# Optimization experiments

Hardware: AMD Instinct MI355X
Metric: run time of the kernel (lower is better)

Reference implementation:

```python
import jax, jax.numpy as jnp
import numpy as np

N = 50000      # nodes
E = 800000     # edges (before self-loops)
IN = 256       # in_dim
HID = 64       # hidden_dim per head
HEADS = 4
OUT = 256      # out_dim
NEG_SLOPE = 0.2


def setup_inputs() -> dict:
    key = jax.random.key(0)
    ks = jax.random.split(key, 12)
    s = 0.1
    return {
        "x": jax.random.normal(ks[0], (N, IN), jnp.float32),
        "edge_index": jax.random.randint(ks[1], (2, E), 0, N, dtype=jnp.int32),
        # layer 1: GATConv(IN, HID, heads=HEADS, concat=True)
        "W1": jax.random.normal(ks[2], (IN, HEADS * HID), jnp.float32) * s,
        "att_src1": jax.random.normal(ks[3], (HEADS, HID), jnp.float32) * s,
        "att_dst1": jax.random.normal(ks[4], (HEADS, HID), jnp.float32) * s,
        "b1": jnp.zeros((HEADS * HID,), jnp.float32),
        # layer 2: GATConv(HEADS*HID, OUT, heads=1, concat=False)
        "W2": jax.random.normal(ks[5], (HEADS * HID, OUT), jnp.float32) * s,
        "att_src2": jax.random.normal(ks[6], (1, OUT), jnp.float32) * s,
        "att_dst2": jax.random.normal(ks[7], (1, OUT), jnp.float32) * s,
        "b2": jnp.zeros((OUT,), jnp.float32),
    }


def _gat_layer(x, src, dst, W, a_src, a_dst, b, heads, concat):
    n = x.shape[0]
    h = (x @ W).reshape(n, heads, -1)                     # [N,H,F]
    al_s = jnp.einsum('nhf,hf->nh', h, a_src)             # [N,H]
    al_d = jnp.einsum('nhf,hf->nh', h, a_dst)
    e = jax.nn.leaky_relu(al_s[src] + al_d[dst], NEG_SLOPE)  # [E,H]
    # segment softmax over incoming edges of each dst node
    m = jax.lax.stop_gradient(jax.ops.segment_max(e, dst, num_segments=n))
    ex = jnp.exp(e - m[dst])
    denom = jax.ops.segment_sum(ex, dst, num_segments=n)
    alpha = ex / (denom[dst] + 1e-16)                     # [E,H]
    out = jax.ops.segment_sum(h[src] * alpha[:, :, None], dst, num_segments=n)  # [N,H,F]
    out = out.reshape(n, -1) if concat else out.mean(axis=1)
    return out + b


def reference(x, edge_index, W1, att_src1, att_dst1, b1, W2, att_src2, att_dst2, b2):
    n = x.shape[0]
    loop = jnp.arange(n, dtype=edge_index.dtype)
    ei = jnp.concatenate([edge_index, jnp.stack([loop, loop])], axis=1)  # add self loops
    src, dst = ei[0], ei[1]
    h = _gat_layer(x, src, dst, W1, att_src1, att_dst1, b1, HEADS, True)
    h = jax.nn.elu(h)
    out = _gat_layer(h, src, dst, W2, att_src2, att_dst2, b2, 1, False)
    return out
```

## Files before the change

kernel.cpp:

```cpp
#include <hip/hip_runtime.h>
#include <math.h>

#define IN_DIM 256
#define FDIM 256
#define HEADS 4
#define NEG 0.2f
#define MAXD 96

typedef __attribute__((ext_vector_type(8))) short bf16x8;
typedef __attribute__((ext_vector_type(8))) unsigned short u16x8;
typedef __attribute__((ext_vector_type(4))) float f32x4;

__device__ __forceinline__ float leaky(float x){ return x > 0.f ? x : NEG * x; }

__device__ __forceinline__ unsigned short f2bf(float f){
  unsigned int u = __float_as_uint(f);
  unsigned int r = u + 0x7fffu + ((u >> 16) & 1u);
  return (unsigned short)(r >> 16);
}
__device__ __forceinline__ float bf2f(unsigned short s){
  return __uint_as_float(((unsigned int)s) << 16);
}

__device__ __forceinline__ float4 bcast4(float4 v){
  return make_float4(__shfl(v.x,0,64), __shfl(v.y,0,64), __shfl(v.z,0,64), __shfl(v.w,0,64));
}
__device__ __forceinline__ float comp4(float4 v, int h){
  return h==0 ? v.x : h==1 ? v.y : h==2 ? v.z : v.w;
}

__device__ __forceinline__ void gld_lds16(const void* g, void* l){
  __builtin_amdgcn_global_load_lds((const __attribute__((address_space(1))) unsigned int*)g,
                                   (__attribute__((address_space(3))) unsigned int*)l, 16, 0, 0);
}

__global__ void k_hist(const int* __restrict__ dst, int* deg, int E){
  int e = blockIdx.x * blockDim.x + threadIdx.x;
  if (e < E) atomicAdd(&deg[dst[e]], 1);
}

__global__ void k_scanA(const int* __restrict__ deg, int* tmp, int* partials, int n){
  __shared__ int sm[256];
  int i = blockIdx.x * 256 + threadIdx.x;
  int v = (i < n) ? deg[i] + 1 : 0;
  sm[threadIdx.x] = v; __syncthreads();
  for (int off = 1; off < 256; off <<= 1){
    int x = (threadIdx.x >= off) ? sm[threadIdx.x - off] : 0;
    __syncthreads();
    sm[threadIdx.x] += x;
    __syncthreads();
  }
  if (i < n) tmp[i] = sm[threadIdx.x];
  if (threadIdx.x == 255) partials[blockIdx.x] = sm[255];
}

__global__ void k_scanB(int* partials, int nb){
  __shared__ int sm[1024];
  int t = threadIdx.x;
  int v = (t < nb) ? partials[t] : 0;
  sm[t] = v; __syncthreads();
  for (int off = 1; off < 1024; off <<= 1){
    int x = (t >= off) ? sm[t - off] : 0;
    __syncthreads();
    sm[t] += x;
    __syncthreads();
  }
  if (t < nb) partials[t] = sm[t] - v;
}

__global__ void k_scanC(const int* __restrict__ tmp, const int* __restrict__ deg,
                        const int* __restrict__ partials, int* rowptr, int n){
  int i = blockIdx.x * blockDim.x + threadIdx.x;
  if (i < n){
    int incl = tmp[i] + partials[i >> 8];
    rowptr[i] = incl - (deg[i] + 1);
    if (i == n - 1) rowptr[n] = incl;
  }
}

__global__ void k_fill(const int* __restrict__ src, const int* __restrict__ dst,
                       const int* __restrict__ rowptr, int* fill, int* col, int E, int n){
  int e = blockIdx.x * blockDim.x + threadIdx.x;
  if (e < E + n){
    int s, d;
    if (e < E){ s = src[e]; d = dst[e]; } else { s = d = e - E; }
    int pos = atomicAdd(&fill[d], 1);
    col[rowptr[d] + pos] = s;
  }
}

__global__ void k_castwt(const float* __restrict__ x, unsigned short* __restrict__ xb, int M, int castBlocks,
                         const float* __restrict__ W1, unsigned short* __restrict__ W1t,
                         const float* __restrict__ W2, unsigned short* __restrict__ W2t){
  int b = blockIdx.x;
  if (b < castBlocks){
    int idx = b * 256 + threadIdx.x;
    int row = idx >> 6;
    float4 v = make_float4(0.f, 0.f, 0.f, 0.f);
    if (row < M) v = *(const float4*)(x + (size_t)idx * 4);
    ushort4 o;
    o.x = f2bf(v.x); o.y = f2bf(v.y); o.z = f2bf(v.z); o.w = f2bf(v.w);
    *(ushort4*)(xb + (size_t)idx * 4) = o;
  } else {
    int bb = b - castBlocks;
    const float* W = (bb < 256) ? W1 : W2;
    unsigned short* Wt = (bb < 256) ? W1t : W2t;
    int nn = bb & 255, k = threadIdx.x;
    Wt[nn * 256 + k] = f2bf(W[k * 256 + nn]);
  }
}

__global__ __launch_bounds__(256) void k_gemm(const unsigned short* __restrict__ A,
                                              const unsigned short* __restrict__ Bt,
                                              unsigned short* __restrict__ C){
  __shared__ __align__(16) unsigned short sh[8192];
  unsigned short* As = sh;
  unsigned short* Bs = sh + 4096;
  int tid = threadIdx.x;
  int lane = tid & 63, wave = tid >> 6;
  int rowBase = blockIdx.x * 128, colBase = blockIdx.y * 128;
  int wr = (wave & 1) * 64, wc = (wave >> 1) * 64;

  f32x4 acc[4][4] = {};
  int c0 = tid, c1 = tid + 256;
  int r0 = c0 >> 2, kc0 = (c0 & 3) * 8;
  int r1 = c1 >> 2, kc1 = (c1 & 3) * 8;
  int m0 = lane & 15, kq = (lane >> 4) * 8;

  for (int k0 = 0; k0 < 256; k0 += 32){
    gld_lds16(A  + (size_t)(rowBase + r0) * 256 + k0 + kc0, (char*)As + c0 * 16);
    gld_lds16(A  + (size_t)(rowBase + r1) * 256 + k0 + kc1, (char*)As + c1 * 16);
    gld_lds16(Bt + (size_t)(colBase + r0) * 256 + k0 + kc0, (char*)Bs + c0 * 16);
    gld_lds16(Bt + (size_t)(colBase + r1) * 256 + k0 + kc1, (char*)Bs + c1 * 16);
    __syncthreads();
    bf16x8 af[4], bfr[4];
    #pragma unroll
    for (int it = 0; it < 4; ++it)
      af[it] = *(const bf16x8*)(As + (wr + it * 16 + m0) * 32 + kq);
    #pragma unroll
    for (int jt = 0; jt < 4; ++jt)
      bfr[jt] = *(const bf16x8*)(Bs + (wc + jt * 16 + m0) * 32 + kq);
    #pragma unroll
    for (int it = 0; it < 4; ++it)
      #pragma unroll
      for (int jt = 0; jt < 4; ++jt)
        acc[it][jt] = __builtin_amdgcn_mfma_f32_16x16x32_bf16(af[it], bfr[jt], acc[it][jt], 0, 0, 0);
    __syncthreads();
  }
  int cq = lane >> 4, cm = lane & 15;
  #pragma unroll
  for (int p = 0; p < 2; ++p){
    if ((wave >> 1) == p){
      #pragma unroll
      for (int it = 0; it < 4; ++it)
        #pragma unroll
        for (int jt = 0; jt < 4; ++jt)
          #pragma unroll
          for (int r = 0; r < 4; ++r)
            sh[(wr + it * 16 + cq * 4 + r) * 64 + jt * 16 + cm] = f2bf(acc[it][jt][r]);
    }
    __syncthreads();
    #pragma unroll
    for (int q = 0; q < 4; ++q){
      int id = tid + q * 256;
      int r = id >> 3, sg = id & 7;
      u16x8 v = *(const u16x8*)(sh + r * 64 + sg * 8);
      *(u16x8*)(C + (size_t)(rowBase + r) * 256 + colBase + p * 64 + sg * 8) = v;
    }
    __syncthreads();
  }
}

__global__ __launch_bounds__(256) void k_al4(const unsigned short* __restrict__ Hb,
                      const float* __restrict__ as_, const float* __restrict__ ad_,
                      float* als, float* ald, int n){
  int wave = threadIdx.x >> 6, lane = threadIdx.x & 63;
  int i = blockIdx.x * 4 + wave; if (i >= n) i = n - 1;
  int f = lane * 4;
  ushort4 hv = *(const ushort4*)(Hb + (size_t)i * FDIM + f);
  float4 av = *(const float4*)(as_ + f);
  float4 dv = *(const float4*)(ad_ + f);
  float h0 = bf2f(hv.x), h1 = bf2f(hv.y), h2 = bf2f(hv.z), h3 = bf2f(hv.w);
  float ps = h0*av.x + h1*av.y + h2*av.z + h3*av.w;
  float pd = h0*dv.x + h1*dv.y + h2*dv.z + h3*dv.w;
  #pragma unroll
  for (int off = 8; off >= 1; off >>= 1){
    ps += __shfl_down(ps, off, 16);
    pd += __shfl_down(pd, off, 16);
  }
  if ((lane & 15) == 0){
    int h = lane >> 4;
    als[i * HEADS + h] = ps; ald[i * HEADS + h] = pd;
  }
}

__global__ __launch_bounds__(256) void k_al1(const unsigned short* __restrict__ Hb,
                      const float* __restrict__ as_, const float* __restrict__ ad_,
                      float* als, float* ald, int n){
  int wave = threadIdx.x >> 6, lane = threadIdx.x & 63;
  int i = blockIdx.x * 4 + wave; if (i >= n) i = n - 1;
  int f = lane * 4;
  ushort4 hv = *(const ushort4*)(Hb + (size_t)i * FDIM + f);
  float4 av = *(const float4*)(as_ + f);
  float4 dv = *(const float4*)(ad_ + f);
  float h0 = bf2f(hv.x), h1 = bf2f(hv.y), h2 = bf2f(hv.z), h3 = bf2f(hv.w);
  float ps = h0*av.x + h1*av.y + h2*av.z + h3*av.w;
  float pd = h0*dv.x + h1*dv.y + h2*dv.z + h3*dv.w;
  #pragma unroll
  for (int off = 32; off >= 1; off >>= 1){
    ps += __shfl_down(ps, off, 64);
    pd += __shfl_down(pd, off, 64);
  }
  if (lane == 0){ als[i] = ps; ald[i] = pd; }
}

__global__ __launch_bounds__(256) void k_agg1(const unsigned short* __restrict__ Hb,
    const float* __restrict__ als, const float* __restrict__ ald,
    const int* __restrict__ rowptr, const int* __restrict__ col,
    const float* __restrict__ b, unsigned short* __restrict__ outb, int n){
  __shared__ __align__(16) int   colS[4][MAXD];
  __shared__ __align__(16) float wS[4][MAXD][4];
  int wave = threadIdx.x >> 6, t = threadIdx.x & 63;
  int i = blockIdx.x * 4 + wave; if (i >= n) i = n - 1;
  int start = rowptr[i];
  int deg = rowptr[i + 1] - start;
  float4 adv = *(const float4*)(ald + (size_t)i * 4);
  bool staged = (deg <= MAXD);

  float4 ls = make_float4(0.f, 0.f, 0.f, 0.f);
  if (staged){
    for (int j = t; j < deg; j += 64){
      int s = col[start + j];
      colS[wave][j] = s;
      float4 a = *(const float4*)(als + (size_t)s * 4);
      float4 w = make_float4(__expf(leaky(a.x + adv.x)), __expf(leaky(a.y + adv.y)),
                             __expf(leaky(a.z + adv.z)), __expf(leaky(a.w + adv.w)));
      *(float4*)(&wS[wave][j][0]) = w;
      ls.x += w.x; ls.y += w.y; ls.z += w.z; ls.w += w.w;
    }
  } else {
    for (int j = t; j < deg; j += 64){
      int s = col[start + j];
      float4 a = *(const float4*)(als + (size_t)s * 4);
      ls.x += __expf(leaky(a.x + adv.x)); ls.y += __expf(leaky(a.y + adv.y));
      ls.z += __expf(leaky(a.z + adv.z)); ls.w += __expf(leaky(a.w + adv.w));
    }
  }
  #pragma unroll
  for (int off = 32; off >= 1; off >>= 1) ls = make_float4(
      ls.x + __shfl_down(ls.x, off, 64), ls.y + __shfl_down(ls.y, off, 64),
      ls.z + __shfl_down(ls.z, off, 64), ls.w + __shfl_down(ls.w, off, 64));
  float4 d4 = bcast4(ls);
  __syncthreads();

  int e2 = t >> 5, l32 = t & 31;
  int h = l32 >> 3, f = l32 * 8;
  float inv = 1.f / (comp4(d4, h) + 1e-16f);
  const unsigned short* Hrow = Hb + f;
  float a0[8] = {0,0,0,0,0,0,0,0}, a1[8] = {0,0,0,0,0,0,0,0};
  if (staged){
    int j = 0;
    for (; j + 3 < deg; j += 4){
      int j0 = j + e2, j1 = j + 2 + e2;
      int s0 = colS[wave][j0], s1 = colS[wave][j1];
      float w0 = wS[wave][j0][h], w1 = wS[wave][j1][h];
      u16x8 h0 = *(const u16x8*)(Hrow + (size_t)s0 * FDIM);
      u16x8 h1 = *(const u16x8*)(Hrow + (size_t)s1 * FDIM);
      #pragma unroll
      for (int k = 0; k < 8; ++k){ a0[k] += bf2f(h0[k]) * w0; a1[k] += bf2f(h1[k]) * w1; }
    }
    for (; j < deg; j += 2){
      int jj = j + e2;
      if (jj < deg){
        int s = colS[wave][jj]; float w = wS[wave][jj][h];
        u16x8 hh = *(const u16x8*)(Hrow + (size_t)s * FDIM);
        #pragma unroll
        for (int k = 0; k < 8; ++k) a0[k] += bf2f(hh[k]) * w;
      }
    }
  } else {
    float adh = comp4(adv, h);
    for (int j = e2; j < deg; j += 2){
      int s = col[start + j];
      float w = __expf(leaky(als[(size_t)s * 4 + h] + adh));
      u16x8 hh = *(const u16x8*)(Hrow + (size_t)s * FDIM);
      #pragma unroll
      for (int k = 0; k < 8; ++k) a0[k] += bf2f(hh[k]) * w;
    }
  }
  float r[8];
  #pragma unroll
  for (int k = 0; k < 8; ++k){
    r[k] = a0[k] + a1[k];
    r[k] += __shfl_down(r[k], 32, 64);
  }
  if (t < 32){
    float4 bA = *(const float4*)(b + f);
    float4 bB = *(const float4*)(b + f + 4);
    float bb[8] = {bA.x, bA.y, bA.z, bA.w, bB.x, bB.y, bB.z, bB.w};
    u16x8 o;
    #pragma unroll
    for (int k = 0; k < 8; ++k){
      float v = r[k] * inv + bb[k];
      v = (v > 0.f) ? v : (__expf(v) - 1.f);
      o[k] = f2bf(v);
    }
    *(u16x8*)(outb + (size_t)i * FDIM + f) = o;
  }
}

__global__ __launch_bounds__(256) void k_agg2(const unsigned short* __restrict__ Hb,
    const float* __restrict__ als, const float* __restrict__ ald,
    const int* __restrict__ rowptr, const int* __restrict__ col,
    const float* __restrict__ b, float* __restrict__ out, int n){
  __shared__ __align__(16) int   colS[4][MAXD];
  __shared__ __align__(16) float wS[4][MAXD];
  int wave = threadIdx.x >> 6, t = threadIdx.x & 63;
  int i = blockIdx.x * 4 + wave; if (i >= n) i = n - 1;
  int start = rowptr[i];
  int deg = rowptr[i + 1] - start;
  float adv = ald[i];
  bool staged = (deg <= MAXD);

  float ls = 0.f;
  if (staged){
    for (int j = t; j < deg; j += 64){
      int s = col[start + j];
      colS[wave][j] = s;
      float w = __expf(leaky(als[s] + adv));
      wS[wave][j] = w;
      ls += w;
    }
  } else {
    for (int j = t; j < deg; j += 64) ls += __expf(leaky(als[col[start + j]] + adv));
  }
  #pragma unroll
  for (int off = 32; off >= 1; off >>= 1) ls += __shfl_down(ls, off, 64);
  float inv = 1.f / (__shfl(ls, 0, 64) + 1e-16f);
  __syncthreads();

  int e2 = t >> 5, l32 = t & 31;
  int f = l32 * 8;
  const unsigned short* Hrow = Hb + f;
  float a0[8] = {0,0,0,0,0,0,0,0}, a1[8] = {0,0,0,0,0,0,0,0};
  if (staged){
    int j = 0;
    for (; j + 3 < deg; j += 4){
      int j0 = j + e2, j1 = j + 2 + e2;
      int s0 = colS[wave][j0], s1 = colS[wave][j1];
      float w0 = wS[wave][j0], w1 = wS[wave][j1];
      u16x8 h0 = *(const u16x8*)(Hrow + (size_t)s0 * FDIM);
      u16x8 h1 = *(const u16x8*)(Hrow + (size_t)s1 * FDIM);
      #pragma unroll
      for (int k = 0; k < 8; ++k){ a0[k] += bf2f(h0[k]) * w0; a1[k] += bf2f(h1[k]) * w1; }
    }
    for (; j < deg; j += 2){
      int jj = j + e2;
      if (jj < deg){
        int s = colS[wave][jj]; float w = wS[wave][jj];
        u16x8 hh = *(const u16x8*)(Hrow + (size_t)s * FDIM);
        #pragma unroll
        for (int k = 0; k < 8; ++k) a0[k] += bf2f(hh[k]) * w;
      }
    }
  } else {
    for (int j = e2; j < deg; j += 2){
      int s = col[start + j];
      float w = __expf(leaky(als[s] + adv));
      u16x8 hh = *(const u16x8*)(Hrow + (size_t)s * FDIM);
      #pragma unroll
      for (int k = 0; k < 8; ++k) a0[k] += bf2f(hh[k]) * w;
    }
  }
  float r[8];
  #pragma unroll
  for (int k = 0; k < 8; ++k){
    r[k] = a0[k] + a1[k];
    r[k] += __shfl_down(r[k], 32, 64);
  }
  if (t < 32){
    float4 bA = *(const float4*)(b + f);
    float4 bB = *(const float4*)(b + f + 4);
    float4 oA = make_float4(r[0]*inv + bA.x, r[1]*inv + bA.y, r[2]*inv + bA.z, r[3]*inv + bA.w);
    float4 oB = make_float4(r[4]*inv + bB.x, r[5]*inv + bB.y, r[6]*inv + bB.z, r[7]*inv + bB.w);
    *(float4*)(out + (size_t)i * FDIM + f) = oA;
    *(float4*)(out + (size_t)i * FDIM + f + 4) = oB;
  }
}

extern "C" void kernel_launch(void* const* d_in, const int* in_sizes, int n_in,
                              void* d_out, int out_size, void* d_ws, size_t ws_size,
                              hipStream_t stream){
  const float* x   = (const float*)d_in[0];
  const int*   ei  = (const int*)d_in[1];
  const float* W1  = (const float*)d_in[2];
  const float* as1 = (const float*)d_in[3];
  const float* ad1 = (const float*)d_in[4];
  const float* b1  = (const float*)d_in[5];
  const float* W2  = (const float*)d_in[6];
  const float* as2 = (const float*)d_in[7];
  const float* ad2 = (const float*)d_in[8];
  const float* b2  = (const float*)d_in[9];
  float* out = (float*)d_out;

  int n = in_sizes[0] / IN_DIM;
  int E = in_sizes[1] / 2;
  int Mpad = (n + 127) & ~127;
  const int* srcIdx = ei;
  const int* dstIdx = ei + E;

  char* ws = (char*)d_ws;
  size_t off = 0;
  auto alloc = [&](size_t bytes) -> void* {
    void* p = ws + off; off += (bytes + 255) & ~(size_t)255; return p;
  };
  unsigned short* bufA = (unsigned short*)alloc((size_t)Mpad * FDIM * 2);
  unsigned short* bufB = (unsigned short*)alloc((size_t)Mpad * FDIM * 2);
  unsigned short* W1t  = (unsigned short*)alloc(256 * 256 * 2);
  unsigned short* W2t  = (unsigned short*)alloc(256 * 256 * 2);
  int*   tmp      = (int*)alloc((size_t)n * 4);
  int*   deg      = (int*)alloc((size_t)n * 4);
  int*   fill     = (int*)alloc((size_t)n * 4);
  int*   rowptr   = (int*)alloc((size_t)(n + 1) * 4);
  int*   partials = (int*)alloc(1024 * 4);
  int*   col      = (int*)alloc((size_t)(E + n) * 4);
  float* als1     = (float*)alloc((size_t)n * HEADS * 4);
  float* ald1     = (float*)alloc((size_t)n * HEADS * 4);
  float* als2     = (float*)alloc((size_t)n * 4);
  float* ald2     = (float*)alloc((size_t)n * 4);
  (void)ws_size;

  int nb = (n + 255) / 256;
  hipMemsetAsync(deg, 0, (size_t)n * 4, stream);
  hipMemsetAsync(fill, 0, (size_t)n * 4, stream);
  k_hist<<<(E + 255) / 256, 256, 0, stream>>>(dstIdx, deg, E);
  k_scanA<<<nb, 256, 0, stream>>>(deg, tmp, partials, n);
  k_scanB<<<1, 1024, 0, stream>>>(partials, nb);
  k_scanC<<<nb, 256, 0, stream>>>(tmp, deg, partials, rowptr, n);
  k_fill<<<(E + n + 255) / 256, 256, 0, stream>>>(srcIdx, dstIdx, rowptr, fill, col, E, n);

  int castBlocks = (Mpad * (FDIM / 4) + 255) / 256;
  k_castwt<<<castBlocks + 512, 256, 0, stream>>>(x, bufA, n, castBlocks, W1, W1t, W2, W2t);

  dim3 gg(Mpad / 128, FDIM / 128);
  int ga = (n + 3) / 4;
  k_gemm<<<gg, 256, 0, stream>>>(bufA, W1t, bufB);
  k_al4<<<ga, 256, 0, stream>>>(bufB, as1, ad1, als1, ald1, n);
  k_agg1<<<ga, 256, 0, stream>>>(bufB, als1, ald1, rowptr, col, b1, bufA, n);
  k_gemm<<<gg, 256, 0, stream>>>(bufA, W2t, bufB);
  k_al1<<<ga, 256, 0, stream>>>(bufB, as2, ad2, als2, ald2, n);
  k_agg2<<<ga, 256, 0, stream>>>(bufB, als2, ald2, rowptr, col, b2, out, n);
}
```

Measured before the change: 393.1 us.

## Fuse CSR build into cooperative kernel, fold attention logits into GEMM, unroll aggregation

```diff
diff --git a/kernel.cpp b/kernel.cpp
--- a/kernel.cpp
+++ b/kernel.cpp
@@ -1,5 +1,8 @@
 #include <hip/hip_runtime.h>
+#include <hip/hip_cooperative_groups.h>
 #include <math.h>
+
+namespace cg = cooperative_groups;
 
 #define IN_DIM 256
 #define FDIM 256
@@ -34,54 +37,82 @@
                                    (__attribute__((address_space(3))) unsigned int*)l, 16, 0, 0);
 }
 
-__global__ void k_hist(const int* __restrict__ dst, int* deg, int E){
-  int e = blockIdx.x * blockDim.x + threadIdx.x;
-  if (e < E) atomicAdd(&deg[dst[e]], 1);
-}
-
-__global__ void k_scanA(const int* __restrict__ deg, int* tmp, int* partials, int n){
+__global__ void k_coop(const float* __restrict__ x, unsigned short* __restrict__ xb,
+                       int castUnits, int M,
+                       const float* __restrict__ W1, unsigned short* __restrict__ W1t,
+                       const float* __restrict__ W2, unsigned short* __restrict__ W2t,
+                       const int* __restrict__ src, const int* __restrict__ dst, int E, int n,
+                       int* deg, int* fill, int* tmp, int* partials, int* rowptr, int* col,
+                       float* als2, float* ald2){
+  cg::grid_group grid = cg::this_grid();
   __shared__ int sm[256];
-  int i = blockIdx.x * 256 + threadIdx.x;
-  int v = (i < n) ? deg[i] + 1 : 0;
-  sm[threadIdx.x] = v; __syncthreads();
-  for (int off = 1; off < 256; off <<= 1){
-    int x = (threadIdx.x >= off) ? sm[threadIdx.x - off] : 0;
-    __syncthreads();
-    sm[threadIdx.x] += x;
-    __syncthreads();
-  }
-  if (i < n) tmp[i] = sm[threadIdx.x];
-  if (threadIdx.x == 255) partials[blockIdx.x] = sm[255];
-}
-
-__global__ void k_scanB(int* partials, int nb){
-  __shared__ int sm[1024];
   int t = threadIdx.x;
-  int v = (t < nb) ? partials[t] : 0;
-  sm[t] = v; __syncthreads();
-  for (int off = 1; off < 1024; off <<= 1){
-    int x = (t >= off) ? sm[t - off] : 0;
-    __syncthreads();
-    sm[t] += x;
-    __syncthreads();
-  }
-  if (t < nb) partials[t] = sm[t] - v;
-}
-
-__global__ void k_scanC(const int* __restrict__ tmp, const int* __restrict__ deg,
-                        const int* __restrict__ partials, int* rowptr, int n){
-  int i = blockIdx.x * blockDim.x + threadIdx.x;
-  if (i < n){
+  int gt = blockIdx.x * 256 + t;
+  const int GSZ = 256 * 256;
+  int nb = (n + 255) >> 8;
+
+  for (int i = gt; i < n; i += GSZ){ deg[i] = 0; fill[i] = 0; als2[i] = 0.f; ald2[i] = 0.f; }
+  for (int u = gt; u < castUnits; u += GSZ){
+    int row = u >> 6;
+    float4 v = make_float4(0.f, 0.f, 0.f, 0.f);
+    if (row < M) v = *(const float4*)(x + (size_t)u * 4);
+    ushort4 o;
+    o.x = f2bf(v.x); o.y = f2bf(v.y); o.z = f2bf(v.z); o.w = f2bf(v.w);
+    *(ushort4*)(xb + (size_t)u * 4) = o;
+  }
+  for (int u = gt; u < 2 * 65536; u += GSZ){
+    const float* W = (u < 65536) ? W1 : W2;
+    unsigned short* Wt = (u < 65536) ? W1t : W2t;
+    int e = u & 65535;
+    int k = e >> 8, nn = e & 255;
+    Wt[nn * 256 + k] = f2bf(W[k * 256 + nn]);
+  }
+  __threadfence();
+  grid.sync();
+
+  for (int e = gt; e < E; e += GSZ) atomicAdd(&deg[dst[e]], 1);
+  __threadfence();
+  grid.sync();
+
+  if (blockIdx.x < nb){
+    int i = blockIdx.x * 256 + t;
+    int v = (i < n) ? deg[i] + 1 : 0;
+    sm[t] = v; __syncthreads();
+    for (int off = 1; off < 256; off <<= 1){
+      int xv = (t >= off) ? sm[t - off] : 0;
+      __syncthreads();
+      sm[t] += xv;
+      __syncthreads();
+    }
+    if (i < n) tmp[i] = sm[t];
+    if (t == 255) partials[blockIdx.x] = sm[255];
+  }
+  __threadfence();
+  grid.sync();
+
+  if (blockIdx.x == 0){
+    int v = (t < nb) ? partials[t] : 0;
+    sm[t] = v; __syncthreads();
+    for (int off = 1; off < 256; off <<= 1){
+      int xv = (t >= off) ? sm[t - off] : 0;
+      __syncthreads();
+      sm[t] += xv;
+      __syncthreads();
+    }
+    if (t < nb) partials[t] = sm[t] - v;
+  }
+  __threadfence();
+  grid.sync();
+
+  for (int i = gt; i < n; i += GSZ){
     int incl = tmp[i] + partials[i >> 8];
     rowptr[i] = incl - (deg[i] + 1);
     if (i == n - 1) rowptr[n] = incl;
   }
-}
-
-__global__ void k_fill(const int* __restrict__ src, const int* __restrict__ dst,
-                       const int* __restrict__ rowptr, int* fill, int* col, int E, int n){
-  int e = blockIdx.x * blockDim.x + threadIdx.x;
-  if (e < E + n){
+  __threadfence();
+  grid.sync();
+
+  for (int e = gt; e < E + n; e += GSZ){
     int s, d;
     if (e < E){ s = src[e]; d = dst[e]; } else { s = d = e - E; }
     int pos = atomicAdd(&fill[d], 1);
@@ -89,30 +120,12 @@
   }
 }
 
-__global__ void k_castwt(const float* __restrict__ x, unsigned short* __restrict__ xb, int M, int castBlocks,
-                         const float* __restrict__ W1, unsigned short* __restrict__ W1t,
-                         const float* __restrict__ W2, unsigned short* __restrict__ W2t){
-  int b = blockIdx.x;
-  if (b < castBlocks){
-    int idx = b * 256 + threadIdx.x;
-    int row = idx >> 6;
-    float4 v = make_float4(0.f, 0.f, 0.f, 0.f);
-    if (row < M) v = *(const float4*)(x + (size_t)idx * 4);
-    ushort4 o;
-    o.x = f2bf(v.x); o.y = f2bf(v.y); o.z = f2bf(v.z); o.w = f2bf(v.w);
-    *(ushort4*)(xb + (size_t)idx * 4) = o;
-  } else {
-    int bb = b - castBlocks;
-    const float* W = (bb < 256) ? W1 : W2;
-    unsigned short* Wt = (bb < 256) ? W1t : W2t;
-    int nn = bb & 255, k = threadIdx.x;
-    Wt[nn * 256 + k] = f2bf(W[k * 256 + nn]);
-  }
-}
-
+template<int L>
 __global__ __launch_bounds__(256) void k_gemm(const unsigned short* __restrict__ A,
                                               const unsigned short* __restrict__ Bt,
-                                              unsigned short* __restrict__ C){
+                                              unsigned short* __restrict__ C,
+                                              const float* __restrict__ avS, const float* __restrict__ avD,
+                                              float* __restrict__ als, float* __restrict__ ald, int nvalid){
   __shared__ __align__(16) unsigned short sh[8192];
   unsigned short* As = sh;
   unsigned short* Bs = sh + 4096;
@@ -160,6 +173,34 @@
             sh[(wr + it * 16 + cq * 4 + r) * 64 + jt * 16 + cm] = f2bf(acc[it][jt][r]);
     }
     __syncthreads();
+    {
+      int r = tid >> 1, half = tid & 1;
+      int rg = rowBase + r;
+      const float* aS;
+      const float* aD;
+      if (L == 1){ aS = avS + (blockIdx.y * 2 + p) * 64; aD = avD + (blockIdx.y * 2 + p) * 64; }
+      else       { aS = avS + colBase + p * 64;          aD = avD + colBase + p * 64; }
+      float ps = 0.f, pd = 0.f;
+      #pragma unroll
+      for (int k4 = 0; k4 < 8; ++k4){
+        ushort4 hv = *(const ushort4*)(sh + r * 64 + half * 32 + k4 * 4);
+        float4 a4 = *(const float4*)(aS + half * 32 + k4 * 4);
+        float4 d4 = *(const float4*)(aD + half * 32 + k4 * 4);
+        ps += bf2f(hv.x)*a4.x + bf2f(hv.y)*a4.y + bf2f(hv.z)*a4.z + bf2f(hv.w)*a4.w;
+        pd += bf2f(hv.x)*d4.x + bf2f(hv.y)*d4.y + bf2f(hv.z)*d4.z + bf2f(hv.w)*d4.w;
+      }
+      ps += __shfl_xor(ps, 1, 64);
+      pd += __shfl_xor(pd, 1, 64);
+      if (half == 0 && rg < nvalid){
+        if (L == 1){
+          als[rg * 4 + blockIdx.y * 2 + p] = ps;
+          ald[rg * 4 + blockIdx.y * 2 + p] = pd;
+        } else {
+          atomicAdd(&als[rg], ps);
+          atomicAdd(&ald[rg], pd);
+        }
+      }
+    }
     #pragma unroll
     for (int q = 0; q < 4; ++q){
       int id = tid + q * 256;
@@ -169,49 +210,6 @@
     }
     __syncthreads();
   }
-}
-
-__global__ __launch_bounds__(256) void k_al4(const unsigned short* __restrict__ Hb,
-                      const float* __restrict__ as_, const float* __restrict__ ad_,
-                      float* als, float* ald, int n){
-  int wave = threadIdx.x >> 6, lane = threadIdx.x & 63;
-  int i = blockIdx.x * 4 + wave; if (i >= n) i = n - 1;
-  int f = lane * 4;
-  ushort4 hv = *(const ushort4*)(Hb + (size_t)i * FDIM + f);
-  float4 av = *(const float4*)(as_ + f);
-  float4 dv = *(const float4*)(ad_ + f);
-  float h0 = bf2f(hv.x), h1 = bf2f(hv.y), h2 = bf2f(hv.z), h3 = bf2f(hv.w);
-  float ps = h0*av.x + h1*av.y + h2*av.z + h3*av.w;
-  float pd = h0*dv.x + h1*dv.y + h2*dv.z + h3*dv.w;
-  #pragma unroll
-  for (int off = 8; off >= 1; off >>= 1){
-    ps += __shfl_down(ps, off, 16);
-    pd += __shfl_down(pd, off, 16);
-  }
-  if ((lane & 15) == 0){
-    int h = lane >> 4;
-    als[i * HEADS + h] = ps; ald[i * HEADS + h] = pd;
-  }
-}
-
-__global__ __launch_bounds__(256) void k_al1(const unsigned short* __restrict__ Hb,
-                      const float* __restrict__ as_, const float* __restrict__ ad_,
-                      float* als, float* ald, int n){
-  int wave = threadIdx.x >> 6, lane = threadIdx.x & 63;
-  int i = blockIdx.x * 4 + wave; if (i >= n) i = n - 1;
-  int f = lane * 4;
-  ushort4 hv = *(const ushort4*)(Hb + (size_t)i * FDIM + f);
-  float4 av = *(const float4*)(as_ + f);
-  float4 dv = *(const float4*)(ad_ + f);
-  float h0 = bf2f(hv.x), h1 = bf2f(hv.y), h2 = bf2f(hv.z), h3 = bf2f(hv.w);
-  float ps = h0*av.x + h1*av.y + h2*av.z + h3*av.w;
-  float pd = h0*dv.x + h1*dv.y + h2*dv.z + h3*dv.w;
-  #pragma unroll
-  for (int off = 32; off >= 1; off >>= 1){
-    ps += __shfl_down(ps, off, 64);
-    pd += __shfl_down(pd, off, 64);
-  }
-  if (lane == 0){ als[i] = ps; ald[i] = pd; }
 }
 
 __global__ __launch_bounds__(256) void k_agg1(const unsigned short* __restrict__ Hb,
@@ -258,16 +256,22 @@
   float inv = 1.f / (comp4(d4, h) + 1e-16f);
   const unsigned short* Hrow = Hb + f;
   float a0[8] = {0,0,0,0,0,0,0,0}, a1[8] = {0,0,0,0,0,0,0,0};
+  float a2[8] = {0,0,0,0,0,0,0,0}, a3[8] = {0,0,0,0,0,0,0,0};
   if (staged){
     int j = 0;
-    for (; j + 3 < deg; j += 4){
-      int j0 = j + e2, j1 = j + 2 + e2;
-      int s0 = colS[wave][j0], s1 = colS[wave][j1];
-      float w0 = wS[wave][j0][h], w1 = wS[wave][j1][h];
+    for (; j + 7 < deg; j += 8){
+      int j0 = j + e2, j1 = j + 2 + e2, j2 = j + 4 + e2, j3 = j + 6 + e2;
+      int s0 = colS[wave][j0], s1 = colS[wave][j1], s2 = colS[wave][j2], s3 = colS[wave][j3];
+      float w0 = wS[wave][j0][h], w1 = wS[wave][j1][h], w2 = wS[wave][j2][h], w3 = wS[wave][j3][h];
       u16x8 h0 = *(const u16x8*)(Hrow + (size_t)s0 * FDIM);
       u16x8 h1 = *(const u16x8*)(Hrow + (size_t)s1 * FDIM);
-      #pragma unroll
-      for (int k = 0; k < 8; ++k){ a0[k] += bf2f(h0[k]) * w0; a1[k] += bf2f(h1[k]) * w1; }
+      u16x8 h2 = *(const u16x8*)(Hrow + (size_t)s2 * FDIM);
+      u16x8 h3 = *(const u16x8*)(Hrow + (size_t)s3 * FDIM);
+      #pragma unroll
+      for (int k = 0; k < 8; ++k){
+        a0[k] += bf2f(h0[k]) * w0; a1[k] += bf2f(h1[k]) * w1;
+        a2[k] += bf2f(h2[k]) * w2; a3[k] += bf2f(h3[k]) * w3;
+      }
     }
     for (; j < deg; j += 2){
       int jj = j + e2;
@@ -291,7 +295,7 @@
   float r[8];
   #pragma unroll
   for (int k = 0; k < 8; ++k){
-    r[k] = a0[k] + a1[k];
+    r[k] = (a0[k] + a1[k]) + (a2[k] + a3[k]);
     r[k] += __shfl_down(r[k], 32, 64);
   }
   if (t < 32){
@@ -343,16 +347,22 @@
   int f = l32 * 8;
   const unsigned short* Hrow = Hb + f;
   float a0[8] = {0,0,0,0,0,0,0,0}, a1[8] = {0,0,0,0,0,0,0,0};
+  float a2[8] = {0,0,0,0,0,0,0,0}, a3[8] = {0,0,0,0,0,0,0,0};
   if (staged){
     int j = 0;
-    for (; j + 3 < deg; j += 4){
-      int j0 = j + e2, j1 = j + 2 + e2;
-      int s0 = colS[wave][j0], s1 = colS[wave][j1];
-      float w0 = wS[wave][j0], w1 = wS[wave][j1];
+    for (; j + 7 < deg; j += 8){
+      int j0 = j + e2, j1 = j + 2 + e2, j2 = j + 4 + e2, j3 = j + 6 + e2;
+      int s0 = colS[wave][j0], s1 = colS[wave][j1], s2 = colS[wave][j2], s3 = colS[wave][j3];
+      float w0 = wS[wave][j0], w1 = wS[wave][j1], w2 = wS[wave][j2], w3 = wS[wave][j3];
       u16x8 h0 = *(const u16x8*)(Hrow + (size_t)s0 * FDIM);
       u16x8 h1 = *(const u16x8*)(Hrow + (size_t)s1 * FDIM);
-      #pragma unroll
-      for (int k = 0; k < 8; ++k){ a0[k] += bf2f(h0[k]) * w0; a1[k] += bf2f(h1[k]) * w1; }
+      u16x8 h2 = *(const u16x8*)(Hrow + (size_t)s2 * FDIM);
+      u16x8 h3 = *(const u16x8*)(Hrow + (size_t)s3 * FDIM);
+      #pragma unroll
+      for (int k = 0; k < 8; ++k){
+        a0[k] += bf2f(h0[k]) * w0; a1[k] += bf2f(h1[k]) * w1;
+        a2[k] += bf2f(h2[k]) * w2; a3[k] += bf2f(h3[k]) * w3;
+      }
     }
     for (; j < deg; j += 2){
       int jj = j + e2;
@@ -375,7 +385,7 @@
   float r[8];
   #pragma unroll
   for (int k = 0; k < 8; ++k){
-    r[k] = a0[k] + a1[k];
+    r[k] = (a0[k] + a1[k]) + (a2[k] + a3[k]);
     r[k] += __shfl_down(r[k], 32, 64);
   }
   if (t < 32){
@@ -422,7 +432,7 @@
   int*   deg      = (int*)alloc((size_t)n * 4);
   int*   fill     = (int*)alloc((size_t)n * 4);
   int*   rowptr   = (int*)alloc((size_t)(n + 1) * 4);
-  int*   partials = (int*)alloc(1024 * 4);
+  int*   partials = (int*)alloc(256 * 4);
   int*   col      = (int*)alloc((size_t)(E + n) * 4);
   float* als1     = (float*)alloc((size_t)n * HEADS * 4);
   float* ald1     = (float*)alloc((size_t)n * HEADS * 4);
@@ -430,24 +440,18 @@
   float* ald2     = (float*)alloc((size_t)n * 4);
   (void)ws_size;
 
-  int nb = (n + 255) / 256;
-  hipMemsetAsync(deg, 0, (size_t)n * 4, stream);
-  hipMemsetAsync(fill, 0, (size_t)n * 4, stream);
-  k_hist<<<(E + 255) / 256, 256, 0, stream>>>(dstIdx, deg, E);
-  k_scanA<<<nb, 256, 0, stream>>>(deg, tmp, partials, n);
-  k_scanB<<<1, 1024, 0, stream>>>(partials, nb);
-  k_scanC<<<nb, 256, 0, stream>>>(tmp, deg, partials, rowptr, n);
-  k_fill<<<(E + n + 255) / 256, 256, 0, stream>>>(srcIdx, dstIdx, rowptr, fill, col, E, n);
-
-  int castBlocks = (Mpad * (FDIM / 4) + 255) / 256;
-  k_castwt<<<castBlocks + 512, 256, 0, stream>>>(x, bufA, n, castBlocks, W1, W1t, W2, W2t);
+  int castUnits = Mpad * (FDIM / 4);
+  void* args[] = { (void*)&x, (void*)&bufA, (void*)&castUnits, (void*)&n,
+                   (void*)&W1, (void*)&W1t, (void*)&W2, (void*)&W2t,
+                   (void*)&srcIdx, (void*)&dstIdx, (void*)&E, (void*)&n,
+                   (void*)&deg, (void*)&fill, (void*)&tmp, (void*)&partials,
+                   (void*)&rowptr, (void*)&col, (void*)&als2, (void*)&ald2 };
+  hipLaunchCooperativeKernel((void*)k_coop, dim3(256), dim3(256), args, 0, stream);
 
   dim3 gg(Mpad / 128, FDIM / 128);
   int ga = (n + 3) / 4;
-  k_gemm<<<gg, 256, 0, stream>>>(bufA, W1t, bufB);
-  k_al4<<<ga, 256, 0, stream>>>(bufB, as1, ad1, als1, ald1, n);
+  k_gemm<1><<<gg, 256, 0, stream>>>(bufA, W1t, bufB, as1, ad1, als1, ald1, n);
   k_agg1<<<ga, 256, 0, stream>>>(bufB, als1, ald1, rowptr, col, b1, bufA, n);
-  k_gemm<<<gg, 256, 0, stream>>>(bufA, W2t, bufB);
-  k_al1<<<ga, 256, 0, stream>>>(bufB, as2, ad2, als2, ald2, n);
+  k_gemm<2><<<gg, 256, 0, stream>>>(bufA, W2t, bufB, as2, ad2, als2, ald2, n);
   k_agg2<<<ga, 256, 0, stream>>>(bufB, als2, ald2, rowptr, col, b2, out, n);
 }
```

Result: slower. 700.6 us (+78.2%).
